# Performance work log

Hardware: AMD Instinct MI355X
Metric: run time of the kernel (lower is better)

The kernel has to match this reference:

```python
import jax, jax.numpy as jnp
import numpy as np

N = 100000          # total nodes
E = 1600000         # edges
C = 128             # in_channels
H = 256             # hidden_size
ACT_DIM = 20        # nodes per graph -> batch = N // ACT_DIM


def setup_inputs() -> dict:
    key = jax.random.key(0)
    ks = jax.random.split(key, 10)
    x = jax.random.normal(ks[0], (N, C), dtype=jnp.float32)
    edge_index = jax.random.randint(ks[1], (2, E), 0, N, dtype=jnp.int64)
    s = 0.05
    conv_w = jax.random.normal(ks[2], (C, C), dtype=jnp.float32) * s   # [in, out]
    conv_b = jnp.zeros((C,), dtype=jnp.float32)
    lin1_w = jax.random.normal(ks[3], (H, C), dtype=jnp.float32) * s   # torch [out, in]
    lin1_b = jnp.zeros((H,), dtype=jnp.float32)
    lin2_w = jax.random.normal(ks[4], (H, H), dtype=jnp.float32) * s
    lin2_b = jnp.zeros((H,), dtype=jnp.float32)
    lin3_w = jax.random.normal(ks[5], (1, H), dtype=jnp.float32) * s
    lin3_b = jnp.zeros((1,), dtype=jnp.float32)
    return {"x": x, "edge_index": edge_index,
            "conv_w": conv_w, "conv_b": conv_b,
            "lin1_w": lin1_w, "lin1_b": lin1_b,
            "lin2_w": lin2_w, "lin2_b": lin2_b,
            "lin3_w": lin3_w, "lin3_b": lin3_b}


def gcn_conv(x, edge_index, w, b):
    """PyG GCNConv: x' = D^{-1/2} (A + I) D^{-1/2} (x W) + b."""
    n = x.shape[0]
    loops = jnp.arange(n, dtype=edge_index.dtype)
    src = jnp.concatenate([edge_index[0], loops])  # [E + N]
    dst = jnp.concatenate([edge_index[1], loops])
    deg = jax.ops.segment_sum(jnp.ones_like(dst, dtype=x.dtype), dst, num_segments=n)
    dinv = jnp.where(deg > 0, jax.lax.rsqrt(deg), 0.0)
    norm = dinv[src] * dinv[dst]                   # [E + N]
    xw = x @ w                                     # [N, out]
    msg = xw[src] * norm[:, None]                  # gather + scale, [E+N, out]
    out = jax.ops.segment_sum(msg, dst, num_segments=n)  # scatter-add
    return out + b


def reference(x, edge_index, conv_w, conv_b, lin1_w, lin1_b, lin2_w, lin2_b, lin3_w, lin3_b):
    out = jax.nn.relu(gcn_conv(x, edge_index, conv_w, conv_b))
    h = out + x                                    # residual, [N, C]
    h = h.reshape(-1, ACT_DIM, C)                  # [B, act_dim, C]
    h = jax.nn.relu(h @ lin1_w.T + lin1_b)         # [B, act_dim, H]
    h = jax.nn.relu(h @ lin2_w.T + lin2_b)
    h = jnp.sum(h, axis=1)                         # [B, H]
    h = h @ lin3_w.T + lin3_b                      # [B, 1]
    if h.shape[0] == 1:                            # torch .squeeze(0) semantics
        h = h[0]
    return h
```

## Files before the change

kernel.cpp:

```cpp
#include <hip/hip_runtime.h>
#include <hip/hip_bf16.h>
#include <cstddef>

#define NNODES 100000
#define NEDGES 1600000
#define CIN 128
#define HID 256
#define ACT 20
#define NGRAPH (NNODES / ACT)
#define BSHIFT 8
#define NB ((NNODES + 255) >> 8)
#define BIN_WGS 512
#define PER_WG (NEDGES / BIN_WGS)
#define CAP 8192
#define CVT_ITEMS 114688
#define CVT_WGS ((CVT_ITEMS + 255) / 256)

typedef __attribute__((ext_vector_type(8))) short short8;
typedef __attribute__((ext_vector_type(4))) float f32x4;
typedef __attribute__((ext_vector_type(2))) float f32x2;
typedef __attribute__((ext_vector_type(4))) unsigned u32x4;

__device__ __forceinline__ unsigned short f2b(float f) {
    unsigned u = __float_as_uint(f);
    u += 0x7FFF + ((u >> 16) & 1);
    return (unsigned short)(u >> 16);
}
__device__ __forceinline__ f32x2 bf2up(unsigned u) {
    f32x2 r;
    r.x = __uint_as_float(u << 16);
    r.y = __uint_as_float(u & 0xffff0000u);
    return r;
}


__global__ __launch_bounds__(256) void bin_k(const int* __restrict__ ei,
                                             int* __restrict__ bfill,
                                             unsigned* __restrict__ entries,
                                             const float* __restrict__ conv_w,
                                             const float* __restrict__ lin1_w,
                                             const float* __restrict__ lin2_w,
                                             unsigned short* __restrict__ wt0,
                                             unsigned short* __restrict__ wt1,
                                             unsigned short* __restrict__ wt2) {
    __shared__ int cnt[NB], lofs[NB], base[NB], cur[NB];
    __shared__ unsigned lbuf[PER_WG];
    __shared__ int gdst[PER_WG];
    __shared__ int wsum[4];
    if (blockIdx.x >= BIN_WGS) {
        int id = (blockIdx.x - BIN_WGS) * 256 + threadIdx.x;
        if (id < 16384) {
            int k = id >> 7, n = id & 127;
            wt0[n * 128 + k] = f2b(conv_w[k * 128 + n]);
        } else if (id < 16384 + 32768) {
            int i = id - 16384;
            wt1[i] = f2b(lin1_w[i]);
        } else if (id < 16384 + 32768 + 65536) {
            int i = id - 49152;
            wt2[i] = f2b(lin2_w[i]);
        }
        return;
    }
    const int t = threadIdx.x;
    for (int i = t; i < NB; i += 256) { cnt[i] = 0; cur[i] = 0; }
    __syncthreads();
    const int s = blockIdx.x * PER_WG;
    const int e = s + PER_WG;
    for (int i = s + t; i < e; i += 256)
        atomicAdd(&cnt[ei[NEDGES + i] >> BSHIFT], 1);
    __syncthreads();
    int c0 = (2 * t < NB) ? cnt[2 * t] : 0;
    int c1 = (2 * t + 1 < NB) ? cnt[2 * t + 1] : 0;
    int v = c0 + c1;
    int lane = t & 63, wid = t >> 6;
    int inc = v;
#pragma unroll
    for (int o = 1; o < 64; o <<= 1) {
        int tv = __shfl_up(inc, o, 64);
        if (lane >= o) inc += tv;
    }
    if (lane == 63) wsum[wid] = inc;
    __syncthreads();
    int woff = 0;
#pragma unroll
    for (int w = 0; w < 4; ++w) woff += (w < wid) ? wsum[w] : 0;
    int excl = inc + woff - v;
    if (2 * t < NB) lofs[2 * t] = excl;
    if (2 * t + 1 < NB) lofs[2 * t + 1] = excl + c0;
    __syncthreads();
    for (int b = t; b < NB; b += 256)
        base[b] = cnt[b] ? atomicAdd(&bfill[b], cnt[b]) : 0;
    __syncthreads();
    for (int i = s + t; i < e; i += 256) {
        int src = ei[i], dst = ei[NEDGES + i];
        int b = dst >> BSHIFT;
        int r = atomicAdd(&cur[b], 1);
        int slot = lofs[b] + r;
        lbuf[slot] = ((unsigned)src << 8) | (unsigned)(dst & 255);
        int g = base[b] + r;
        gdst[slot] = (g < CAP) ? (int)((size_t)b * CAP + g) : -1;
    }
    __syncthreads();
    for (int i = t; i < PER_WG; i += 256) {
        int g = gdst[i];
        if (g >= 0) entries[g] = lbuf[i];
    }
}


__global__ __launch_bounds__(256) void bucket_build_k(
    const unsigned* __restrict__ entries, const int* __restrict__ bfill,
    int2* __restrict__ rowptr2, int* __restrict__ csr, float* __restrict__ dinv) {
    const int b = blockIdx.x;
    const int count = min(bfill[b], CAP);
    const int node0 = b << BSHIFT;
    const int nn = min(256, NNODES - node0);
    const size_t gbase = (size_t)b * CAP;
    __shared__ int cnt[256], off[256], cur[256];
    __shared__ int wsum[4];
    __shared__ int sbuf[CAP];
    const int t = threadIdx.x;
    cnt[t] = 0; cur[t] = 0;
    __syncthreads();
    for (int i = t; i < count; i += 256)
        atomicAdd(&cnt[entries[gbase + i] & 255], 1);
    __syncthreads();
    int lane = t & 63, wid = t >> 6;
    int v = cnt[t];
    int inc = v;
#pragma unroll
    for (int o = 1; o < 64; o <<= 1) {
        int tv = __shfl_up(inc, o, 64);
        if (lane >= o) inc += tv;
    }
    if (lane == 63) wsum[wid] = inc;
    __syncthreads();
    int woff = 0;
#pragma unroll
    for (int w = 0; w < 4; ++w) woff += (w < wid) ? wsum[w] : 0;
    int excl = inc + woff - v;
    off[t] = excl;
    if (t < nn) {
        rowptr2[node0 + t] = make_int2((int)gbase + excl, (int)gbase + excl + v);
        dinv[node0 + t] = rsqrtf(1.0f + (float)v);
    }
    __syncthreads();
    for (int i = t; i < count; i += 256) {
        unsigned en = entries[gbase + i];
        int loc = (int)(en & 255);
        int r = atomicAdd(&cur[loc], 1);
        sbuf[off[loc] + r] = (int)(en >> 8);
    }
    __syncthreads();
    const int c4 = count >> 2;
    const int4* sb4 = reinterpret_cast<const int4*>(sbuf);
    int4* cs4 = reinterpret_cast<int4*>(csr + gbase);
    for (int i = t; i < c4; i += 256) cs4[i] = sb4[i];
    for (int i = (c4 << 2) + t; i < count; i += 256) csr[gbase + i] = sbuf[i];
}


__global__ __launch_bounds__(256) void mgemm0_k(
    const float* __restrict__ Af, const unsigned short* __restrict__ B,
    const float* __restrict__ dinv, unsigned short* __restrict__ Cout, int M)
{
    const int tid = threadIdx.x;
    const int wid = tid >> 6;
    const int lane = tid & 63;
    const int quad = lane >> 4;
    const int l16 = lane & 15;
    const int bm = blockIdx.x * 128 + (wid >> 1) * 64;
    const int bn = (wid & 1) * 64;

    const float* pa[4];
    const unsigned short* pb[4];
#pragma unroll
    for (int t = 0; t < 4; ++t) {
        int m = bm + t * 16 + l16; if (m >= M) m = M - 1;
        pa[t] = Af + (size_t)m * 128 + quad * 8;
        int n = bn + t * 16 + l16;
        pb[t] = B + (size_t)n * 128 + quad * 8;
    }

    f32x4 acc[4][4];
#pragma unroll
    for (int i = 0; i < 4; ++i)
#pragma unroll
        for (int j = 0; j < 4; ++j) {
            f32x4 z = {0.f, 0.f, 0.f, 0.f};
            acc[i][j] = z;
        }

    float4 afl[2][4][2];
    short8 bf[2][4];
#pragma unroll
    for (int t = 0; t < 4; ++t) {
        afl[0][t][0] = *reinterpret_cast<const float4*>(pa[t]);
        afl[0][t][1] = *reinterpret_cast<const float4*>(pa[t] + 4);
        bf[0][t] = *reinterpret_cast<const short8*>(pb[t]);
    }

#pragma unroll
    for (int kt = 0; kt < 4; ++kt) {
        const int cur = kt & 1, nxt = cur ^ 1;
        if (kt < 3) {
#pragma unroll
            for (int t = 0; t < 4; ++t) {
                afl[nxt][t][0] = *reinterpret_cast<const float4*>(pa[t] + (kt + 1) * 32);
                afl[nxt][t][1] = *reinterpret_cast<const float4*>(pa[t] + (kt + 1) * 32 + 4);
                bf[nxt][t] = *reinterpret_cast<const short8*>(pb[t] + (kt + 1) * 32);
            }
        }
        short8 a[4];
#pragma unroll
        for (int t = 0; t < 4; ++t) {
            float4 f0 = afl[cur][t][0], f1 = afl[cur][t][1];
            short8 av;
            av[0] = (short)f2b(f0.x); av[1] = (short)f2b(f0.y);
            av[2] = (short)f2b(f0.z); av[3] = (short)f2b(f0.w);
            av[4] = (short)f2b(f1.x); av[5] = (short)f2b(f1.y);
            av[6] = (short)f2b(f1.z); av[7] = (short)f2b(f1.w);
            a[t] = av;
        }
#pragma unroll
        for (int i = 0; i < 4; ++i)
#pragma unroll
            for (int j = 0; j < 4; ++j)
                acc[i][j] = __builtin_amdgcn_mfma_f32_16x16x32_bf16(a[i], bf[cur][j], acc[i][j], 0, 0, 0);
    }

#pragma unroll
    for (int i = 0; i < 4; ++i)
#pragma unroll
        for (int r = 0; r < 4; ++r) {
            int row = bm + i * 16 + quad * 4 + r;
            if (row >= M) continue;
            float dv = dinv[row];
#pragma unroll
            for (int j = 0; j < 4; ++j) {
                int col = bn + j * 16 + l16;
                Cout[(size_t)row * 128 + col] = f2b(acc[i][j][r] * dv);
            }
        }
}


__global__ __launch_bounds__(256) void gather_k(
    const int2* __restrict__ rowptr2, const int* __restrict__ csr,
    const unsigned short* __restrict__ xws, const float* __restrict__ dinv,
    const float* __restrict__ x, const float* __restrict__ conv_b,
    unsigned short* __restrict__ h0)
{
    const int node = blockIdx.x * 4 + (threadIdx.x >> 6);
    if (node >= NNODES) return;
    const int lane = threadIdx.x & 63;
    const int sub = lane >> 4;
    const int c16 = lane & 15;

    const int2 se = rowptr2[node];
    const int start = se.x, end = se.y;

    f32x2 a[4];
    if (sub == 0) {
        u32x4 v = *reinterpret_cast<const u32x4*>(xws + (size_t)node * CIN + c16 * 8);
        a[0] = bf2up(v.x); a[1] = bf2up(v.y); a[2] = bf2up(v.z); a[3] = bf2up(v.w);
    } else {
        f32x2 z = {0.f, 0.f};
        a[0] = z; a[1] = z; a[2] = z; a[3] = z;
    }

    const int es = start & ~3;
    for (int q = es; q < end; q += 16) {
        const int b0 = q + sub * 4;
        const u32x4 ic = *reinterpret_cast<const u32x4*>(csr + b0);
        u32x4 r[4];
        bool val[4];
#pragma unroll
        for (int j = 0; j < 4; ++j) {
            const int e = b0 + j;
            const bool ok = (e >= start) & (e < end);
            const int idx = ok ? (int)ic[j] : node;
            r[j] = *reinterpret_cast<const u32x4*>(xws + (size_t)idx * CIN + c16 * 8);
            val[j] = ok;
        }
#pragma unroll
        for (int j = 0; j < 4; ++j)
            if (val[j]) {
                a[0] += bf2up(r[j].x); a[1] += bf2up(r[j].y);
                a[2] += bf2up(r[j].z); a[3] += bf2up(r[j].w);
            }
    }

#pragma unroll
    for (int k = 0; k < 4; ++k) {
        a[k].x += __shfl_xor(a[k].x, 16, 64);
        a[k].y += __shfl_xor(a[k].y, 16, 64);
        a[k].x += __shfl_xor(a[k].x, 32, 64);
        a[k].y += __shfl_xor(a[k].y, 32, 64);
    }

    if (sub == 0) {
        const float dv = dinv[node];
        const float4 b0v = *reinterpret_cast<const float4*>(conv_b + c16 * 8);
        const float4 b1v = *reinterpret_cast<const float4*>(conv_b + c16 * 8 + 4);
        const float4 x0 = *reinterpret_cast<const float4*>(x + (size_t)node * CIN + c16 * 8);
        const float4 x1 = *reinterpret_cast<const float4*>(x + (size_t)node * CIN + c16 * 8 + 4);
        float o[8];
        o[0] = fmaxf(a[0].x * dv + b0v.x, 0.f) + x0.x;
        o[1] = fmaxf(a[0].y * dv + b0v.y, 0.f) + x0.y;
        o[2] = fmaxf(a[1].x * dv + b0v.z, 0.f) + x0.z;
        o[3] = fmaxf(a[1].y * dv + b0v.w, 0.f) + x0.w;
        o[4] = fmaxf(a[2].x * dv + b1v.x, 0.f) + x1.x;
        o[5] = fmaxf(a[2].y * dv + b1v.y, 0.f) + x1.y;
        o[6] = fmaxf(a[3].x * dv + b1v.z, 0.f) + x1.z;
        o[7] = fmaxf(a[3].y * dv + b1v.w, 0.f) + x1.w;
        u32x4 pk;
        pk.x = (unsigned)f2b(o[0]) | ((unsigned)f2b(o[1]) << 16);
        pk.y = (unsigned)f2b(o[2]) | ((unsigned)f2b(o[3]) << 16);
        pk.z = (unsigned)f2b(o[4]) | ((unsigned)f2b(o[5]) << 16);
        pk.w = (unsigned)f2b(o[6]) | ((unsigned)f2b(o[7]) << 16);
        *reinterpret_cast<u32x4*>(h0 + (size_t)node * CIN + c16 * 8) = pk;
    }
}


__global__ __launch_bounds__(256, 2) void fmlp_k(
    const unsigned short* __restrict__ h0, const unsigned short* __restrict__ w1,
    const float* __restrict__ b1, const unsigned short* __restrict__ w2,
    const float* __restrict__ b2, const float* __restrict__ w3,
    float* __restrict__ rowsum, int M)
{
    __shared__ unsigned short h1s[64 * 256];
    __shared__ unsigned short h0s[64 * 128];
    const int tid = threadIdx.x;
    const int wave = tid >> 6;
    const int lane = tid & 63;
    const int quad = lane >> 4;
    const int l16 = lane & 15;
    const int bm = blockIdx.x * 64;
    const int nc0 = wave * 64;

    {
        typedef __attribute__((address_space(1))) const unsigned short* gp_t;
        typedef __attribute__((address_space(3))) unsigned short* lp_t;
#pragma unroll
        for (int p = 0; p < 4; ++p) {
            const int L = p * 256 + tid;
            const int r = L >> 4, sc = L & 15;
            const int c = (sc & 8) | ((sc ^ r) & 7);
            const unsigned short* gsrc = h0 + (size_t)(bm + r) * 128 + c * 8;
            __builtin_amdgcn_global_load_lds((gp_t)gsrc,
                (lp_t)(h0s + (size_t)(p * 256 + wave * 64) * 8), 16, 0, 0);
        }
    }

    f32x4 acc[4][4];
#pragma unroll
    for (int i = 0; i < 4; ++i)
#pragma unroll
        for (int j = 0; j < 4; ++j) {
            f32x4 z = {0.f, 0.f, 0.f, 0.f};
            acc[i][j] = z;
        }

    __syncthreads();

    {
        const unsigned short* pb[4];
#pragma unroll
        for (int t = 0; t < 4; ++t) {
            int n = nc0 + t * 16 + l16;
            pb[t] = w1 + (size_t)n * 128 + quad * 8;
        }
        short8 af[2][4], bf[2][4];
#pragma unroll
        for (int t = 0; t < 4; ++t) {
            const int row = t * 16 + l16;
            const int c = quad;
            const int pos = (c & 8) | ((c ^ row) & 7);
            af[0][t] = *reinterpret_cast<const short8*>(&h0s[row * 128 + pos * 8]);
            bf[0][t] = *reinterpret_cast<const short8*>(pb[t]);
        }
#pragma unroll
        for (int kt = 0; kt < 4; ++kt) {
            const int cur = kt & 1, nxt = cur ^ 1;
            if (kt < 3) {
#pragma unroll
                for (int t = 0; t < 4; ++t) {
                    const int row = t * 16 + l16;
                    const int c = (kt + 1) * 4 + quad;
                    const int pos = (c & 8) | ((c ^ row) & 7);
                    af[nxt][t] = *reinterpret_cast<const short8*>(&h0s[row * 128 + pos * 8]);
                    bf[nxt][t] = *reinterpret_cast<const short8*>(pb[t] + (kt + 1) * 32);
                }
            }
#pragma unroll
            for (int i = 0; i < 4; ++i)
#pragma unroll
                for (int j = 0; j < 4; ++j)
                    acc[i][j] = __builtin_amdgcn_mfma_f32_16x16x32_bf16(af[cur][i], bf[cur][j], acc[i][j], 0, 0, 0);
        }
#pragma unroll
        for (int nt = 0; nt < 4; ++nt) {
            int col = nc0 + nt * 16 + l16;
            float bv = b1[col];
            int chunk = col >> 3, rem = col & 7;
#pragma unroll
            for (int mt = 0; mt < 4; ++mt)
#pragma unroll
                for (int r = 0; r < 4; ++r) {
                    int row = mt * 16 + quad * 4 + r;
                    h1s[row * 256 + (((chunk ^ (row & 7)) << 3) | rem)] =
                        f2b(fmaxf(acc[mt][nt][r] + bv, 0.f));
                }
        }
    }
    __syncthreads();

#pragma unroll
    for (int i = 0; i < 4; ++i)
#pragma unroll
        for (int j = 0; j < 4; ++j) {
            f32x4 z = {0.f, 0.f, 0.f, 0.f};
            acc[i][j] = z;
        }
    {
        const unsigned short* pb[4];
#pragma unroll
        for (int t = 0; t < 4; ++t) {
            int n = nc0 + t * 16 + l16;
            pb[t] = w2 + (size_t)n * 256 + quad * 8;
        }
        short8 af[3][4], bf[3][4];
#pragma unroll
        for (int t = 0; t < 4; ++t) {
            int row = t * 16 + l16;
            af[0][t] = *reinterpret_cast<const short8*>(
                &h1s[row * 256 + ((quad ^ (row & 7)) << 3)]);
            af[1][t] = *reinterpret_cast<const short8*>(
                &h1s[row * 256 + (((4 + quad) ^ (row & 7)) << 3)]);
            bf[0][t] = *reinterpret_cast<const short8*>(pb[t]);
            bf[1][t] = *reinterpret_cast<const short8*>(pb[t] + 32);
        }
#pragma unroll
        for (int kt = 0; kt < 8; ++kt) {
            const int cu = kt % 3, nx = (kt + 2) % 3;
            if (kt + 2 < 8) {
                const int c2 = (kt + 2) * 4 + quad;
#pragma unroll
                for (int t = 0; t < 4; ++t) {
                    int row = t * 16 + l16;
                    af[nx][t] = *reinterpret_cast<const short8*>(
                        &h1s[row * 256 + ((c2 ^ (row & 7)) << 3)]);
                    bf[nx][t] = *reinterpret_cast<const short8*>(pb[t] + (kt + 2) * 32);
                }
            }
#pragma unroll
            for (int i = 0; i < 4; ++i)
#pragma unroll
                for (int j = 0; j < 4; ++j)
                    acc[i][j] = __builtin_amdgcn_mfma_f32_16x16x32_bf16(af[cu][i], bf[cu][j], acc[i][j], 0, 0, 0);
        }
    }

    float part[4][4];
#pragma unroll
    for (int mt = 0; mt < 4; ++mt)
#pragma unroll
        for (int r = 0; r < 4; ++r) part[mt][r] = 0.f;
#pragma unroll
    for (int nt = 0; nt < 4; ++nt) {
        int col = nc0 + nt * 16 + l16;
        float bs = b2[col];
        float wv3 = w3[col];
#pragma unroll
        for (int mt = 0; mt < 4; ++mt)
#pragma unroll
            for (int r = 0; r < 4; ++r)
                part[mt][r] += fmaxf(acc[mt][nt][r] + bs, 0.f) * wv3;
    }
#pragma unroll
    for (int mt = 0; mt < 4; ++mt)
#pragma unroll
        for (int r = 0; r < 4; ++r) {
            float v = part[mt][r];
            v += __shfl_xor(v, 1, 64);
            v += __shfl_xor(v, 2, 64);
            v += __shfl_xor(v, 4, 64);
            v += __shfl_xor(v, 8, 64);
            part[mt][r] = v;
        }
    if (l16 == 0) {
#pragma unroll
        for (int mt = 0; mt < 4; ++mt)
#pragma unroll
            for (int r = 0; r < 4; ++r) {
                int row = bm + mt * 16 + quad * 4 + r;
                if (row < M) rowsum[(size_t)row * 4 + wave] = part[mt][r];
            }
    }
}


__global__ __launch_bounds__(256) void final_k(
    const float* __restrict__ rowsum, const float* __restrict__ b3,
    float* __restrict__ out)
{
    int g = blockIdx.x * 256 + threadIdx.x;
    if (g >= NGRAPH) return;
    const float4* p = reinterpret_cast<const float4*>(rowsum + (size_t)g * 80);
    float s = 0.f;
#pragma unroll
    for (int i = 0; i < 20; ++i) {
        float4 v = p[i];
        s += (v.x + v.y) + (v.z + v.w);
    }
    out[g] = s + b3[0];
}


extern "C" void kernel_launch(void* const* d_in, const int* in_sizes, int n_in,
                              void* d_out, int out_size, void* d_ws, size_t ws_size,
                              hipStream_t stream)
{
    const float* x      = (const float*)d_in[0];
    const int*   ei     = (const int*)  d_in[1];
    const float* conv_w = (const float*)d_in[2];
    const float* conv_b = (const float*)d_in[3];
    const float* lin1_w = (const float*)d_in[4];
    const float* lin1_b = (const float*)d_in[5];
    const float* lin2_w = (const float*)d_in[6];
    const float* lin2_b = (const float*)d_in[7];
    const float* lin3_w = (const float*)d_in[8];
    const float* lin3_b = (const float*)d_in[9];
    float* out = (float*)d_out;

    unsigned short* xws     = (unsigned short*)d_ws;
    unsigned short* h0      = xws + (size_t)(NNODES + 8) * 128;
    unsigned*       entries = (unsigned*)(h0 + (size_t)NNODES * 128);
    int*            csr     = (int*)(entries + (size_t)NB * CAP);
    int2*           rowptr2 = (int2*)(csr + (size_t)NB * CAP);
    float*          dinv    = (float*)(rowptr2 + NNODES);
    int*            bfill   = (int*)(dinv + NNODES);
    unsigned short* wt0     = (unsigned short*)(bfill + NB + 8);
    unsigned short* wt1     = wt0 + 16384;
    unsigned short* wt2     = wt1 + 32768;
    float*          rowsum  = (float*)(wt2 + 65536);

    hipMemsetAsync(bfill, 0, NB * sizeof(int), stream);
    bin_k<<<BIN_WGS + CVT_WGS, 256, 0, stream>>>(ei, bfill, entries,
                                                 conv_w, lin1_w, lin2_w,
                                                 wt0, wt1, wt2);
    bucket_build_k<<<NB, 256, 0, stream>>>(entries, bfill, rowptr2, csr, dinv);

    mgemm0_k<<<(NNODES + 127) / 128, 256, 0, stream>>>(x, wt0, dinv, xws, NNODES);

    gather_k<<<(NNODES + 3) / 4, 256, 0, stream>>>(rowptr2, csr, xws, dinv, x, conv_b, h0);

    fmlp_k<<<(NNODES + 63) / 64, 256, 0, stream>>>(h0, wt1, lin1_b, wt2, lin2_b, lin3_w,
                                                   rowsum, NNODES);

    final_k<<<(NGRAPH + 255) / 256, 256, 0, stream>>>(rowsum, lin3_b, out);
}
```

Baseline: 280.5 us.

## Pre-convert x to bf16 in bin kernel and stage A tiles via LDS

Moves the fp32-to-bf16 conversion of x into extra workgroups of the binning kernel, writing into the h0 scratch buffer. The first GEMM then reads bf16 rows with global_load_lds into a swizzled shared-memory tile instead of loading fp32 and converting in registers, and gains a launch bound of two blocks per CU. This halves the GEMM's A-operand read and drops the in-loop conversion, but adds a separate full pass that reads x and writes it back as bf16, plus 32KB of LDS per block. The last block's tile loads are not bounds-checked, so they can read past the end of the converted rows.

```diff
diff --git a/kernel.cpp b/kernel.cpp
--- a/kernel.cpp
+++ b/kernel.cpp
@@ -13,7 +13,9 @@
 #define BIN_WGS 512
 #define PER_WG (NEDGES / BIN_WGS)
 #define CAP 8192
-#define CVT_ITEMS 114688
+#define XCVT_BASE 114688
+#define XCVT_ITEMS 1600000
+#define CVT_ITEMS (XCVT_BASE + XCVT_ITEMS)
 #define CVT_WGS ((CVT_ITEMS + 255) / 256)
 
 typedef __attribute__((ext_vector_type(8))) short short8;
@@ -40,9 +42,11 @@
                                              const float* __restrict__ conv_w,
                                              const float* __restrict__ lin1_w,
                                              const float* __restrict__ lin2_w,
+                                             const float* __restrict__ x,
                                              unsigned short* __restrict__ wt0,
                                              unsigned short* __restrict__ wt1,
-                                             unsigned short* __restrict__ wt2) {
+                                             unsigned short* __restrict__ wt2,
+                                             unsigned short* __restrict__ xbf) {
     __shared__ int cnt[NB], lofs[NB], base[NB], cur[NB];
     __shared__ unsigned lbuf[PER_WG];
     __shared__ int gdst[PER_WG];
@@ -58,6 +62,16 @@
         } else if (id < 16384 + 32768 + 65536) {
             int i = id - 49152;
             wt2[i] = f2b(lin2_w[i]);
+        } else if (id < CVT_ITEMS) {
+            size_t b8 = (size_t)(id - XCVT_BASE) * 8;
+            const float4* xp = reinterpret_cast<const float4*>(x + b8);
+            float4 f0 = xp[0], f1 = xp[1];
+            short8 o;
+            o[0] = (short)f2b(f0.x); o[1] = (short)f2b(f0.y);
+            o[2] = (short)f2b(f0.z); o[3] = (short)f2b(f0.w);
+            o[4] = (short)f2b(f1.x); o[5] = (short)f2b(f1.y);
+            o[6] = (short)f2b(f1.z); o[7] = (short)f2b(f1.w);
+            *reinterpret_cast<short8*>(xbf + b8) = o;
         }
         return;
     }
@@ -160,10 +174,11 @@
 }
 
 
-__global__ __launch_bounds__(256) void mgemm0_k(
-    const float* __restrict__ Af, const unsigned short* __restrict__ B,
+__global__ __launch_bounds__(256, 2) void mgemm0_k(
+    const unsigned short* __restrict__ Abf, const unsigned short* __restrict__ B,
     const float* __restrict__ dinv, unsigned short* __restrict__ Cout, int M)
 {
+    __shared__ unsigned short xbs[128 * 128];
     const int tid = threadIdx.x;
     const int wid = tid >> 6;
     const int lane = tid & 63;
@@ -171,13 +186,25 @@
     const int l16 = lane & 15;
     const int bm = blockIdx.x * 128 + (wid >> 1) * 64;
     const int bn = (wid & 1) * 64;
-
-    const float* pa[4];
+    const int wave = wid;
+
+    {
+        typedef __attribute__((address_space(1))) const unsigned short* gp_t;
+        typedef __attribute__((address_space(3))) unsigned short* lp_t;
+#pragma unroll
+        for (int p = 0; p < 8; ++p) {
+            const int L = p * 256 + tid;
+            const int r = L >> 4, sc = L & 15;
+            const int c = (sc & 8) | ((sc ^ r) & 7);
+            const unsigned short* gsrc = Abf + (size_t)(blockIdx.x * 128 + r) * 128 + c * 8;
+            __builtin_amdgcn_global_load_lds((gp_t)gsrc,
+                (lp_t)(xbs + (size_t)(p * 256 + wave * 64) * 8), 16, 0, 0);
+        }
+    }
+
     const unsigned short* pb[4];
 #pragma unroll
     for (int t = 0; t < 4; ++t) {
-        int m = bm + t * 16 + l16; if (m >= M) m = M - 1;
-        pa[t] = Af + (size_t)m * 128 + quad * 8;
         int n = bn + t * 16 + l16;
         pb[t] = B + (size_t)n * 128 + quad * 8;
     }
@@ -191,12 +218,15 @@
             acc[i][j] = z;
         }
 
-    float4 afl[2][4][2];
-    short8 bf[2][4];
+    __syncthreads();
+
+    short8 af[2][4], bf[2][4];
 #pragma unroll
     for (int t = 0; t < 4; ++t) {
-        afl[0][t][0] = *reinterpret_cast<const float4*>(pa[t]);
-        afl[0][t][1] = *reinterpret_cast<const float4*>(pa[t] + 4);
+        const int row = (wid >> 1) * 64 + t * 16 + l16;
+        const int c = quad;
+        const int pos = (c & 8) | ((c ^ row) & 7);
+        af[0][t] = *reinterpret_cast<const short8*>(&xbs[row * 128 + pos * 8]);
         bf[0][t] = *reinterpret_cast<const short8*>(pb[t]);
     }
 
@@ -206,27 +236,18 @@
         if (kt < 3) {
 #pragma unroll
             for (int t = 0; t < 4; ++t) {
-                afl[nxt][t][0] = *reinterpret_cast<const float4*>(pa[t] + (kt + 1) * 32);
-                afl[nxt][t][1] = *reinterpret_cast<const float4*>(pa[t] + (kt + 1) * 32 + 4);
+                const int row = (wid >> 1) * 64 + t * 16 + l16;
+                const int c = (kt + 1) * 4 + quad;
+                const int pos = (c & 8) | ((c ^ row) & 7);
+                af[nxt][t] = *reinterpret_cast<const short8*>(&xbs[row * 128 + pos * 8]);
                 bf[nxt][t] = *reinterpret_cast<const short8*>(pb[t] + (kt + 1) * 32);
             }
         }
-        short8 a[4];
-#pragma unroll
-        for (int t = 0; t < 4; ++t) {
-            float4 f0 = afl[cur][t][0], f1 = afl[cur][t][1];
-            short8 av;
-            av[0] = (short)f2b(f0.x); av[1] = (short)f2b(f0.y);
-            av[2] = (short)f2b(f0.z); av[3] = (short)f2b(f0.w);
-            av[4] = (short)f2b(f1.x); av[5] = (short)f2b(f1.y);
-            av[6] = (short)f2b(f1.z); av[7] = (short)f2b(f1.w);
-            a[t] = av;
-        }
 #pragma unroll
         for (int i = 0; i < 4; ++i)
 #pragma unroll
             for (int j = 0; j < 4; ++j)
-                acc[i][j] = __builtin_amdgcn_mfma_f32_16x16x32_bf16(a[i], bf[cur][j], acc[i][j], 0, 0, 0);
+                acc[i][j] = __builtin_amdgcn_mfma_f32_16x16x32_bf16(af[cur][i], bf[cur][j], acc[i][j], 0, 0, 0);
     }
 
 #pragma unroll
@@ -549,11 +570,11 @@
 
     hipMemsetAsync(bfill, 0, NB * sizeof(int), stream);
     bin_k<<<BIN_WGS + CVT_WGS, 256, 0, stream>>>(ei, bfill, entries,
-                                                 conv_w, lin1_w, lin2_w,
-                                                 wt0, wt1, wt2);
+                                                 conv_w, lin1_w, lin2_w, x,
+                                                 wt0, wt1, wt2, h0);
     bucket_build_k<<<NB, 256, 0, stream>>>(entries, bfill, rowptr2, csr, dinv);
 
-    mgemm0_k<<<(NNODES + 127) / 128, 256, 0, stream>>>(x, wt0, dinv, xws, NNODES);
+    mgemm0_k<<<(NNODES + 127) / 128, 256, 0, stream>>>(h0, wt0, dinv, xws, NNODES);
 
     gather_k<<<(NNODES + 3) / 4, 256, 0, stream>>>(rowptr2, csr, xws, dinv, x, conv_b, h0);
 
```

Measured after the change: 277.0 us, median of 3. About the same (-1.3%).
